# Performance work log

Hardware: AMD Instinct MI355X
Metric: run time of the kernel (lower is better)

The kernel has to match this reference:

```python
import jax, jax.numpy as jnp
import numpy as np

N_NODES = 50000
N_EDGES = 1600000
D = 128


def setup_inputs() -> dict:
    key = jax.random.key(0)
    ks = jax.random.split(key, 8)
    features = jax.random.normal(ks[0], (N_NODES, D), dtype=jnp.float32)
    edge_src = jax.random.randint(ks[1], (N_EDGES,), 0, N_NODES, dtype=jnp.int32)
    edge_dst = jax.random.randint(ks[2], (N_EDGES,), 0, N_NODES, dtype=jnp.int32)
    edge_weight = jax.random.uniform(ks[3], (N_EDGES,), dtype=jnp.float32)
    scale = 1.0 / np.sqrt(D)
    W1 = jax.random.normal(ks[4], (D, D), dtype=jnp.float32) * scale
    b1 = jnp.zeros((D,), dtype=jnp.float32)
    W2 = jax.random.normal(ks[5], (D, D), dtype=jnp.float32) * scale
    b2 = jnp.zeros((D,), dtype=jnp.float32)
    return {"features": features, "edge_src": edge_src, "edge_dst": edge_dst,
            "edge_weight": edge_weight, "W1": W1, "b1": b1, "W2": W2, "b2": b2}


def _gcn_layer(x, W, b, edge_src, edge_dst, edge_weight, n_nodes):
    # support = X @ W  (dense projection), then spmm: out[d] += w_e * support[s]
    support = x @ W  # [N, D]
    msgs = support[edge_src] * edge_weight[:, None]  # [E, D] gather + scale
    out = jax.ops.segment_sum(msgs, edge_dst, num_segments=n_nodes)  # scatter-add
    return out + b


def reference(features, edge_src, edge_dst, edge_weight, W1, b1, W2, b2):
    h = _gcn_layer(features, W1, b1, edge_src, edge_dst, edge_weight, N_NODES)
    h = jax.nn.relu(h)
    # dropout is identity in eval mode (training=False)
    out = _gcn_layer(h, W2, b2, edge_src, edge_dst, edge_weight, N_NODES)
    return out
```

## Files before the change

kernel.cpp:

```cpp
#include <hip/hip_runtime.h>
#include <hip/hip_fp16.h>
#include <math.h>

#define D 128
#define BSHIFT 7
#define BSIZE (1 << BSHIFT)
#define CHUNK 4096
#define BT 1024
#define CAP 7168
#define BSTR 16
#define LDP 132
#define SENTV 0xFFFFFFFFu

typedef _Float16 half8 __attribute__((ext_vector_type(8)));
typedef float f32x4 __attribute__((ext_vector_type(4)));
typedef float f32x2 __attribute__((ext_vector_type(2)));

#if __has_builtin(__builtin_amdgcn_cvt_pk_f32_fp8) && \
    __has_builtin(__builtin_amdgcn_cvt_pk_fp8_f32)
#define HAVE_FP8_CVT 1
#endif

__device__ __forceinline__ float dec_e4m3(unsigned int b) {
    const unsigned int e = (b >> 3) & 0xF;
    const unsigned int m = b & 7;
    float v;
    if (e == 0) v = (float)m * 0.001953125f;
    else        v = (float)(8 + m) * __uint_as_float((e + 117) << 23);
    return (b & 0x80) ? -v : v;
}

__device__ __forceinline__ unsigned char enc_fp8(float x) {
#ifdef HAVE_FP8_CVT
    return (unsigned char)(__builtin_amdgcn_cvt_pk_fp8_f32(x, x, 0, false) & 0xFF);
#else
    const float ax0 = fabsf(x);
    const unsigned int s = (x < 0.f) ? 0x80u : 0u;
    const float ax = fminf(ax0, 448.0f);
    if (ax < 0.015625f) {
        const int m = __float2int_rn(ax * 512.0f);
        return (unsigned char)(s | (unsigned int)m);
    }
    int ex;
    const float fr = frexpf(ax, &ex);
    int m = __float2int_rn(fr * 16.0f) - 8;
    int e = ex - 1 + 7;
    if (m == 8) { m = 0; e += 1; }
    if (e > 15) return (unsigned char)(s | 0x7E);
    return (unsigned char)(s | ((unsigned int)e << 3) | (unsigned int)m);
#endif
}

__global__ __launch_bounds__(512) void init_misc(int* __restrict__ bcur, int NB,
                                                 const float* __restrict__ W1,
                                                 const float* __restrict__ W2,
                                                 __half* __restrict__ W1t,
                                                 __half* __restrict__ W2t) {
    if (blockIdx.x == 0) {
        const int b = threadIdx.x;
        if (b < NB) bcur[b * BSTR] = b * CAP;
        return;
    }
    const int which = blockIdx.x - 1;
    const float* W = which ? W2 : W1;
    __half* Wt = which ? W2t : W1t;
    for (int i = threadIdx.x; i < D * D; i += 512) {
        const int n = i >> 7, k = i & 127;
        Wt[i] = __float2half(W[k * D + n]);
    }
}

__device__ __forceinline__ void gemm_body_f32(const float* __restrict__ X,
                                              const __half* __restrict__ Wt,
                                              unsigned char* __restrict__ Y,
                                              int M, int bx) {
    const int lane = threadIdx.x & 63;
    const int wv = threadIdx.x >> 6;
    const int row0 = bx * 256 + wv * 16;
    const int m = lane & 15;
    const int q = lane >> 4;

    if (row0 >= M) return;
    const int rsafe = min(row0 + m, M - 1);
    const float4* Xr = (const float4*)(X + (size_t)rsafe * D);
    half8 a[4];
#pragma unroll
    for (int kt = 0; kt < 4; ++kt) {
        const float4 lo = Xr[kt * 8 + q * 2];
        const float4 hi = Xr[kt * 8 + q * 2 + 1];
        a[kt] = (half8){(_Float16)lo.x, (_Float16)lo.y, (_Float16)lo.z,
                        (_Float16)lo.w, (_Float16)hi.x, (_Float16)hi.y,
                        (_Float16)hi.z, (_Float16)hi.w};
    }

    const half8* WT8 = (const half8*)Wt;
#pragma unroll
    for (int ct = 0; ct < 8; ++ct) {
        const int n = ct * 16 + m;
        f32x4 acc = {0.f, 0.f, 0.f, 0.f};
#pragma unroll
        for (int kt = 0; kt < 4; ++kt) {
            const half8 b = WT8[(size_t)n * 16 + kt * 4 + q];
            acc = __builtin_amdgcn_mfma_f32_16x16x32_f16(a[kt], b, acc, 0, 0, 0);
        }
#pragma unroll
        for (int r = 0; r < 4; ++r) {
            const int orow = row0 + q * 4 + r;
            if (orow < M)
                Y[(size_t)orow * D + ct * 16 + m] = enc_fp8(acc[r]);
        }
    }
}

__global__ __launch_bounds__(BT) void scatter_gemm1(const int* __restrict__ src,
                                                    const int* __restrict__ dst,
                                                    const float* __restrict__ wgt,
                                                    int* __restrict__ bcur,
                                                    unsigned int* __restrict__ csrA,
                                                    int E, int NB, int nscat,
                                                    const float* __restrict__ X,
                                                    const __half* __restrict__ W1t,
                                                    unsigned char* __restrict__ sup,
                                                    int M) {
    if (blockIdx.x >= (unsigned)nscat) {
        gemm_body_f32(X, W1t, sup, M, blockIdx.x - nscat);
        return;
    }
    __shared__ int lhist[512];
    __shared__ int lstart[512];
    __shared__ int lcur[512];
    const int tid = threadIdx.x;
    const int base = blockIdx.x * CHUNK;

    for (int b = tid; b < NB; b += BT) lhist[b] = 0;
    __syncthreads();

    int dreg[CHUNK / BT];
#pragma unroll
    for (int u = 0; u < CHUNK / BT; ++u) {
        const int e = base + u * BT + tid;
        dreg[u] = (e < E) ? dst[e] : -1;
        if (dreg[u] >= 0) atomicAdd(&lhist[dreg[u] >> BSHIFT], 1);
    }
    __syncthreads();

    for (int b = tid; b < NB; b += BT) {
        const int c = lhist[b];
        if (c) {
            const int r = atomicAdd(&bcur[b * BSTR], (c + 15) & ~15);
            lstart[b] = r;
            lcur[b] = r;
        }
    }
    __syncthreads();

#pragma unroll
    for (int u = 0; u < CHUNK / BT; ++u) {
        const int d = dreg[u];
        if (d >= 0) {
            const int e = base + u * BT + tid;
            const int b = d >> BSHIFT;
            const int pos = atomicAdd(&lcur[b], 1);
            const unsigned int wq =
                (unsigned int)__float2int_rn(wgt[e] * 511.0f);
            const unsigned int kv = (unsigned int)src[e] |
                                    ((unsigned int)(d & (BSIZE - 1)) << 16) |
                                    (wq << 23);
            if (pos < (b + 1) * CAP) csrA[pos] = kv;
        }
    }
    __syncthreads();

    for (int b = tid; b < NB; b += BT) {
        const int c = lhist[b];
        if (c) {
            const int beg = lstart[b] + c;
            const int fin = lstart[b] + ((c + 15) & ~15);
            for (int p = beg; p < fin; ++p)
                if (p < (b + 1) * CAP) csrA[p] = SENTV;
        }
    }
}

__device__ __forceinline__ void accum8(float acc[8], uint2 raw, float w) {
#ifdef HAVE_FP8_CVT
    const f32x2 f01 = __builtin_amdgcn_cvt_pk_f32_fp8(raw.x, false);
    const f32x2 f23 = __builtin_amdgcn_cvt_pk_f32_fp8(raw.x, true);
    const f32x2 f45 = __builtin_amdgcn_cvt_pk_f32_fp8(raw.y, false);
    const f32x2 f67 = __builtin_amdgcn_cvt_pk_f32_fp8(raw.y, true);
    acc[0] = fmaf(w, f01[0], acc[0]);
    acc[1] = fmaf(w, f01[1], acc[1]);
    acc[2] = fmaf(w, f23[0], acc[2]);
    acc[3] = fmaf(w, f23[1], acc[3]);
    acc[4] = fmaf(w, f45[0], acc[4]);
    acc[5] = fmaf(w, f45[1], acc[5]);
    acc[6] = fmaf(w, f67[0], acc[6]);
    acc[7] = fmaf(w, f67[1], acc[7]);
#else
#pragma unroll
    for (int i = 0; i < 4; ++i)
        acc[i] = fmaf(w, dec_e4m3((raw.x >> (8 * i)) & 0xFF), acc[i]);
#pragma unroll
    for (int i = 0; i < 4; ++i)
        acc[4 + i] = fmaf(w, dec_e4m3((raw.y >> (8 * i)) & 0xFF), acc[4 + i]);
#endif
}

__device__ __forceinline__ float kv_w(unsigned int kv) {
    return (float)(kv >> 23) * (1.0f / 511.0f);
}

__device__ __forceinline__ void gather_row(const uint2* __restrict__ supv,
                                           const unsigned int* __restrict__ csr,
                                           int beg, int end, int l, float acc[8]) {
    int j = beg;
    for (; j + 16 <= end; j += 16) {
        unsigned int kv[16];
        uint2 r[16];
#pragma unroll
        for (int u = 0; u < 16; ++u) kv[u] = csr[j + u];
#pragma unroll
        for (int u = 0; u < 16; ++u)
            r[u] = supv[(size_t)(kv[u] & 0xFFFF) * 16 + l];
#pragma unroll
        for (int u = 0; u < 16; ++u) accum8(acc, r[u], kv_w(kv[u]));
    }
    if (j + 8 <= end) {
        unsigned int kv[8];
        uint2 r[8];
#pragma unroll
        for (int u = 0; u < 8; ++u) kv[u] = csr[j + u];
#pragma unroll
        for (int u = 0; u < 8; ++u)
            r[u] = supv[(size_t)(kv[u] & 0xFFFF) * 16 + l];
#pragma unroll
        for (int u = 0; u < 8; ++u) accum8(acc, r[u], kv_w(kv[u]));
        j += 8;
    }
    if (j + 4 <= end) {
        unsigned int kv[4];
        uint2 r[4];
#pragma unroll
        for (int u = 0; u < 4; ++u) kv[u] = csr[j + u];
#pragma unroll
        for (int u = 0; u < 4; ++u)
            r[u] = supv[(size_t)(kv[u] & 0xFFFF) * 16 + l];
#pragma unroll
        for (int u = 0; u < 4; ++u) accum8(acc, r[u], kv_w(kv[u]));
        j += 4;
    }
    for (; j < end; ++j) {
        const unsigned int kv = csr[j];
        const uint2 r = supv[(size_t)(kv & 0xFFFF) * 16 + l];
        accum8(acc, r, kv_w(kv));
    }
}

__device__ __forceinline__ void gather_row_lds(const uint2* __restrict__ supv,
                                               const unsigned int* ekv2,
                                               int beg, int end, int l, float acc[8]) {
    int j = beg;
    for (; j + 16 <= end; j += 16) {
        unsigned int kv[16];
        uint2 r[16];
#pragma unroll
        for (int u = 0; u < 16; ++u) kv[u] = ekv2[j + u];
#pragma unroll
        for (int u = 0; u < 16; ++u)
            r[u] = supv[(size_t)(kv[u] & 0xFFFF) * 16 + l];
#pragma unroll
        for (int u = 0; u < 16; ++u) accum8(acc, r[u], kv_w(kv[u]));
    }
    if (j + 8 <= end) {
        unsigned int kv[8];
        uint2 r[8];
#pragma unroll
        for (int u = 0; u < 8; ++u) kv[u] = ekv2[j + u];
#pragma unroll
        for (int u = 0; u < 8; ++u)
            r[u] = supv[(size_t)(kv[u] & 0xFFFF) * 16 + l];
#pragma unroll
        for (int u = 0; u < 8; ++u) accum8(acc, r[u], kv_w(kv[u]));
        j += 8;
    }
    if (j + 4 <= end) {
        unsigned int kv[4];
        uint2 r[4];
#pragma unroll
        for (int u = 0; u < 4; ++u) kv[u] = ekv2[j + u];
#pragma unroll
        for (int u = 0; u < 4; ++u)
            r[u] = supv[(size_t)(kv[u] & 0xFFFF) * 16 + l];
#pragma unroll
        for (int u = 0; u < 4; ++u) accum8(acc, r[u], kv_w(kv[u]));
        j += 4;
    }
    for (; j < end; ++j) {
        const unsigned int kv = ekv2[j];
        const uint2 r = supv[(size_t)(kv & 0xFFFF) * 16 + l];
        accum8(acc, r, kv_w(kv));
    }
}

__global__ __launch_bounds__(BT) void gather_sort_gemm(
    const unsigned int* __restrict__ csrA, const int* __restrict__ bcur,
    int* __restrict__ offsets, int* __restrict__ deg,
    unsigned int* __restrict__ csr,
    const unsigned char* __restrict__ sup, const float* __restrict__ b1,
    const __half* __restrict__ W2t, unsigned char* __restrict__ sup2, int M) {
    __shared__ unsigned int ekv2[CAP];
    __shared__ _Float16 hA[BSIZE * LDP];
    __shared__ int hist[BSIZE];
    __shared__ int loff[BSIZE];
    __shared__ int ldeg[BSIZE];
    __shared__ int ncur[BSIZE];
    __shared__ int wtot[2];

    const int b = blockIdx.x;
    const int n0 = b << BSHIFT;
    const int tid = threadIdx.x;
    const int nloc = min(BSIZE, M - n0);
    const int bstart = b * CAP;
    const int bend = min(bcur[b * BSTR], bstart + CAP);

    if (tid < BSIZE) hist[tid] = 0;
    __syncthreads();

    unsigned int reg[CAP / BT];
#pragma unroll
    for (int i = 0; i < CAP / BT; ++i) {
        const int j = bstart + i * BT + tid;
        unsigned int kv = SENTV;
        if (j < bend) kv = csrA[j];
        reg[i] = kv;
        if ((kv & 0xFFFFu) != 0xFFFFu)
            atomicAdd(&hist[(kv >> 16) & (BSIZE - 1)], 1);
    }
    __syncthreads();

    const int lane = tid & 63;
    const int wv = tid >> 6;
    const int v = (tid < BSIZE) ? hist[tid] : 0;
    int incl = v;
#pragma unroll
    for (int off = 1; off < 64; off <<= 1) {
        int t = __shfl_up(incl, off, 64);
        if (lane >= off) incl += t;
    }
    if (tid < BSIZE && lane == 63) wtot[wv] = incl;
    __syncthreads();
    if (tid < BSIZE) {
        const int carry = (wv == 1) ? wtot[0] : 0;
        const int ex = incl - v + carry;
        loff[tid] = ex;
        ldeg[tid] = v;
        ncur[tid] = ex;
        if (tid < nloc) {
            offsets[n0 + tid] = bstart + ex;
            deg[n0 + tid] = v;
        }
    }
    for (int i = tid; i < (BSIZE - nloc) * LDP; i += BT)
        hA[nloc * LDP + i] = (_Float16)0.f;
    __syncthreads();

#pragma unroll
    for (int i = 0; i < CAP / BT; ++i) {
        const unsigned int kv = reg[i];
        if ((kv & 0xFFFFu) != 0xFFFFu) {
            const int pos = atomicAdd(&ncur[(kv >> 16) & (BSIZE - 1)], 1);
            ekv2[pos] = kv;
        }
    }
    __syncthreads();

#pragma unroll
    for (int i = 0; i < CAP / BT; ++i)
        csr[bstart + i * BT + tid] = ekv2[i * BT + tid];

    const int grp = tid >> 4;
    const int l = tid & 15;
    const uint2* supv = (const uint2*)sup;
    const float4 c0 = ((const float4*)b1)[l * 2];
    const float4 c1 = ((const float4*)b1)[l * 2 + 1];
    for (int n = grp; n < nloc; n += 64) {
        float acc[8];
        acc[0] = c0.x; acc[1] = c0.y; acc[2] = c0.z; acc[3] = c0.w;
        acc[4] = c1.x; acc[5] = c1.y; acc[6] = c1.z; acc[7] = c1.w;
        const int beg = loff[n];
        gather_row_lds(supv, ekv2, beg, beg + ldeg[n], l, acc);
        half8 hv;
#pragma unroll
        for (int i = 0; i < 8; ++i) hv[i] = (_Float16)fmaxf(acc[i], 0.f);
        *(half8*)&hA[n * LDP + l * 8] = hv;
    }
    __syncthreads();

    const int m = lane & 15;
    const int qq = lane >> 4;
    const int rt = wv >> 1;
    const int ct0 = (wv & 1) * 4;
    half8 a[4];
#pragma unroll
    for (int kt = 0; kt < 4; ++kt)
        a[kt] = *(const half8*)&hA[(rt * 16 + m) * LDP + kt * 32 + qq * 8];

    const half8* WT8 = (const half8*)W2t;
#pragma unroll
    for (int c = 0; c < 4; ++c) {
        const int ct = ct0 + c;
        const int ncol = ct * 16 + m;
        f32x4 dacc = {0.f, 0.f, 0.f, 0.f};
#pragma unroll
        for (int kt = 0; kt < 4; ++kt) {
            const half8 bb = WT8[(size_t)ncol * 16 + kt * 4 + qq];
            dacc = __builtin_amdgcn_mfma_f32_16x16x32_f16(a[kt], bb, dacc, 0, 0, 0);
        }
#pragma unroll
        for (int r = 0; r < 4; ++r) {
            const int orow = n0 + rt * 16 + qq * 4 + r;
            if (orow < M)
                sup2[(size_t)orow * D + ct * 16 + m] = enc_fp8(dacc[r]);
        }
    }
}

__global__ __launch_bounds__(256) void gather_out(const unsigned char* __restrict__ sup,
                                                  const int* __restrict__ offsets,
                                                  const int* __restrict__ deg,
                                                  const unsigned int* __restrict__ csr,
                                                  const float* __restrict__ bias,
                                                  float* __restrict__ out, int M) {
    const int tid = threadIdx.x;
    const int q = tid >> 4;
    const int l = tid & 15;
    const int n = blockIdx.x * 16 + q;
    if (n >= M) return;

    float acc[8];
    {
        const float4 c0 = ((const float4*)bias)[l * 2];
        const float4 c1 = ((const float4*)bias)[l * 2 + 1];
        acc[0] = c0.x; acc[1] = c0.y; acc[2] = c0.z; acc[3] = c0.w;
        acc[4] = c1.x; acc[5] = c1.y; acc[6] = c1.z; acc[7] = c1.w;
    }
    const int beg = offsets[n];
    gather_row((const uint2*)sup, csr, beg, beg + deg[n], l, acc);

    f32x4* out4 = (f32x4*)out;
    const f32x4 o0 = {acc[0], acc[1], acc[2], acc[3]};
    const f32x4 o1 = {acc[4], acc[5], acc[6], acc[7]};
    __builtin_nontemporal_store(o0, out4 + (size_t)n * 32 + l * 2);
    __builtin_nontemporal_store(o1, out4 + (size_t)n * 32 + l * 2 + 1);
}

extern "C" void kernel_launch(void* const* d_in, const int* in_sizes, int n_in,
                              void* d_out, int out_size, void* d_ws, size_t ws_size,
                              hipStream_t stream) {
    const float* features = (const float*)d_in[0];
    const int*   esrc     = (const int*)d_in[1];
    const int*   edst     = (const int*)d_in[2];
    const float* ew       = (const float*)d_in[3];
    const float* W1       = (const float*)d_in[4];
    const float* b1       = (const float*)d_in[5];
    const float* W2       = (const float*)d_in[6];
    const float* b2       = (const float*)d_in[7];
    float* out = (float*)d_out;

    const int M = in_sizes[0] / D;
    const int E = in_sizes[1];
    const int NB = (M + BSIZE - 1) >> BSHIFT;

    unsigned int* csrA = (unsigned int*)d_ws;
    unsigned int* csr  = csrA + (size_t)NB * CAP;
    unsigned char* sup = (unsigned char*)(csr + (size_t)NB * CAP);
    unsigned char* sup2 = sup + (size_t)M * D;
    int*    offsets = (int*)(sup2 + (size_t)M * D);
    int*    deg     = offsets + M;
    int*    bcur    = deg + M;
    __half* W1t     = (__half*)(bcur + (size_t)NB * BSTR);
    __half* W2t     = W1t + D * D;

    const int gemmb = (M + 255) / 256;
    const int node_blocks = (M + 15) / 16;
    const int nscat = (E + CHUNK - 1) / CHUNK;

    init_misc<<<3, 512, 0, stream>>>(bcur, NB, W1, W2, W1t, W2t);
    scatter_gemm1<<<nscat + gemmb, BT, 0, stream>>>(esrc, edst, ew, bcur, csrA, E,
                                                    NB, nscat, features, W1t, sup, M);
    gather_sort_gemm<<<NB, BT, 0, stream>>>(csrA, bcur, offsets, deg, csr, sup, b1,
                                            W2t, sup2, M);
    gather_out<<<node_blocks, 256, 0, stream>>>(sup2, offsets, deg, csr, b2, out, M);
}
```

Measured before the change: 244.6 us.

## Split second-layer support into column slabs and unfuse scatter from gemm1

Layer-2 support is now stored as two 64-column fp8 slabs, and the final gather runs per slab, each block handling 32 nodes with 8 lanes per node. Each slab is 3.2MB instead of 6.4MB, so the random gathers should stay in cache better. The fused scatter+gemm1 kernel is also split into two launches, with gemm1 using 64-row blocks of 256 threads. The cost is an extra launch, loss of overlap between scatter and gemm, and reading the CSR indices twice in the final gather.

```diff
diff --git a/kernel.cpp b/kernel.cpp
--- a/kernel.cpp
+++ b/kernel.cpp
@@ -10,6 +10,7 @@
 #define CAP 7168
 #define BSTR 16
 #define LDP 132
+#define SLW 64
 #define SENTV 0xFFFFFFFFu
 
 typedef _Float16 half8 __attribute__((ext_vector_type(8)));
@@ -70,62 +71,12 @@
     }
 }
 
-__device__ __forceinline__ void gemm_body_f32(const float* __restrict__ X,
-                                              const __half* __restrict__ Wt,
-                                              unsigned char* __restrict__ Y,
-                                              int M, int bx) {
-    const int lane = threadIdx.x & 63;
-    const int wv = threadIdx.x >> 6;
-    const int row0 = bx * 256 + wv * 16;
-    const int m = lane & 15;
-    const int q = lane >> 4;
-
-    if (row0 >= M) return;
-    const int rsafe = min(row0 + m, M - 1);
-    const float4* Xr = (const float4*)(X + (size_t)rsafe * D);
-    half8 a[4];
-#pragma unroll
-    for (int kt = 0; kt < 4; ++kt) {
-        const float4 lo = Xr[kt * 8 + q * 2];
-        const float4 hi = Xr[kt * 8 + q * 2 + 1];
-        a[kt] = (half8){(_Float16)lo.x, (_Float16)lo.y, (_Float16)lo.z,
-                        (_Float16)lo.w, (_Float16)hi.x, (_Float16)hi.y,
-                        (_Float16)hi.z, (_Float16)hi.w};
-    }
-
-    const half8* WT8 = (const half8*)Wt;
-#pragma unroll
-    for (int ct = 0; ct < 8; ++ct) {
-        const int n = ct * 16 + m;
-        f32x4 acc = {0.f, 0.f, 0.f, 0.f};
-#pragma unroll
-        for (int kt = 0; kt < 4; ++kt) {
-            const half8 b = WT8[(size_t)n * 16 + kt * 4 + q];
-            acc = __builtin_amdgcn_mfma_f32_16x16x32_f16(a[kt], b, acc, 0, 0, 0);
-        }
-#pragma unroll
-        for (int r = 0; r < 4; ++r) {
-            const int orow = row0 + q * 4 + r;
-            if (orow < M)
-                Y[(size_t)orow * D + ct * 16 + m] = enc_fp8(acc[r]);
-        }
-    }
-}
-
-__global__ __launch_bounds__(BT) void scatter_gemm1(const int* __restrict__ src,
-                                                    const int* __restrict__ dst,
-                                                    const float* __restrict__ wgt,
-                                                    int* __restrict__ bcur,
-                                                    unsigned int* __restrict__ csrA,
-                                                    int E, int NB, int nscat,
-                                                    const float* __restrict__ X,
-                                                    const __half* __restrict__ W1t,
-                                                    unsigned char* __restrict__ sup,
-                                                    int M) {
-    if (blockIdx.x >= (unsigned)nscat) {
-        gemm_body_f32(X, W1t, sup, M, blockIdx.x - nscat);
-        return;
-    }
+__global__ __launch_bounds__(BT) void scatter_prep(const int* __restrict__ src,
+                                                   const int* __restrict__ dst,
+                                                   const float* __restrict__ wgt,
+                                                   int* __restrict__ bcur,
+                                                   unsigned int* __restrict__ csrA,
+                                                   int E, int NB) {
     __shared__ int lhist[512];
     __shared__ int lstart[512];
     __shared__ int lcur[512];
@@ -178,6 +129,47 @@
             const int fin = lstart[b] + ((c + 15) & ~15);
             for (int p = beg; p < fin; ++p)
                 if (p < (b + 1) * CAP) csrA[p] = SENTV;
+        }
+    }
+}
+
+__global__ __launch_bounds__(256) void gemm1(const float* __restrict__ X,
+                                             const __half* __restrict__ Wt,
+                                             unsigned char* __restrict__ Y, int M) {
+    const int lane = threadIdx.x & 63;
+    const int wv = threadIdx.x >> 6;
+    const int row0 = blockIdx.x * 64 + wv * 16;
+    const int m = lane & 15;
+    const int q = lane >> 4;
+
+    if (row0 >= M) return;
+    const int rsafe = min(row0 + m, M - 1);
+    const float4* Xr = (const float4*)(X + (size_t)rsafe * D);
+    half8 a[4];
+#pragma unroll
+    for (int kt = 0; kt < 4; ++kt) {
+        const float4 lo = Xr[kt * 8 + q * 2];
+        const float4 hi = Xr[kt * 8 + q * 2 + 1];
+        a[kt] = (half8){(_Float16)lo.x, (_Float16)lo.y, (_Float16)lo.z,
+                        (_Float16)lo.w, (_Float16)hi.x, (_Float16)hi.y,
+                        (_Float16)hi.z, (_Float16)hi.w};
+    }
+
+    const half8* WT8 = (const half8*)Wt;
+#pragma unroll
+    for (int ct = 0; ct < 8; ++ct) {
+        const int n = ct * 16 + m;
+        f32x4 acc = {0.f, 0.f, 0.f, 0.f};
+#pragma unroll
+        for (int kt = 0; kt < 4; ++kt) {
+            const half8 b = WT8[(size_t)n * 16 + kt * 4 + q];
+            acc = __builtin_amdgcn_mfma_f32_16x16x32_f16(a[kt], b, acc, 0, 0, 0);
+        }
+#pragma unroll
+        for (int r = 0; r < 4; ++r) {
+            const int orow = row0 + q * 4 + r;
+            if (orow < M)
+                Y[(size_t)orow * D + ct * 16 + m] = enc_fp8(acc[r]);
         }
     }
 }
@@ -210,52 +202,6 @@
     return (float)(kv >> 23) * (1.0f / 511.0f);
 }
 
-__device__ __forceinline__ void gather_row(const uint2* __restrict__ supv,
-                                           const unsigned int* __restrict__ csr,
-                                           int beg, int end, int l, float acc[8]) {
-    int j = beg;
-    for (; j + 16 <= end; j += 16) {
-        unsigned int kv[16];
-        uint2 r[16];
-#pragma unroll
-        for (int u = 0; u < 16; ++u) kv[u] = csr[j + u];
-#pragma unroll
-        for (int u = 0; u < 16; ++u)
-            r[u] = supv[(size_t)(kv[u] & 0xFFFF) * 16 + l];
-#pragma unroll
-        for (int u = 0; u < 16; ++u) accum8(acc, r[u], kv_w(kv[u]));
-    }
-    if (j + 8 <= end) {
-        unsigned int kv[8];
-        uint2 r[8];
-#pragma unroll
-        for (int u = 0; u < 8; ++u) kv[u] = csr[j + u];
-#pragma unroll
-        for (int u = 0; u < 8; ++u)
-            r[u] = supv[(size_t)(kv[u] & 0xFFFF) * 16 + l];
-#pragma unroll
-        for (int u = 0; u < 8; ++u) accum8(acc, r[u], kv_w(kv[u]));
-        j += 8;
-    }
-    if (j + 4 <= end) {
-        unsigned int kv[4];
-        uint2 r[4];
-#pragma unroll
-        for (int u = 0; u < 4; ++u) kv[u] = csr[j + u];
-#pragma unroll
-        for (int u = 0; u < 4; ++u)
-            r[u] = supv[(size_t)(kv[u] & 0xFFFF) * 16 + l];
-#pragma unroll
-        for (int u = 0; u < 4; ++u) accum8(acc, r[u], kv_w(kv[u]));
-        j += 4;
-    }
-    for (; j < end; ++j) {
-        const unsigned int kv = csr[j];
-        const uint2 r = supv[(size_t)(kv & 0xFFFF) * 16 + l];
-        accum8(acc, r, kv_w(kv));
-    }
-}
-
 __device__ __forceinline__ void gather_row_lds(const uint2* __restrict__ supv,
                                                const unsigned int* ekv2,
                                                int beg, int end, int l, float acc[8]) {
@@ -299,6 +245,51 @@
         const unsigned int kv = ekv2[j];
         const uint2 r = supv[(size_t)(kv & 0xFFFF) * 16 + l];
         accum8(acc, r, kv_w(kv));
+    }
+}
+
+__device__ __forceinline__ void gather_row_sl(const uint2* __restrict__ supv,
+                                              const unsigned int* __restrict__ csr,
+                                              int beg, int end, int p, float acc[8]) {
+    int j = beg;
+    for (; j + 16 <= end; j += 16) {
+        unsigned int kv[16];
+        uint2 r[16];
+#pragma unroll
+        for (int u = 0; u < 16; ++u) kv[u] = csr[j + u];
+#pragma unroll
+        for (int u = 0; u < 16; ++u)
+            r[u] = supv[(size_t)(kv[u] & 0xFFFF) * 8 + p];
+#pragma unroll
+        for (int u = 0; u < 16; ++u) accum8(acc, r[u], kv_w(kv[u]));
+    }
+    if (j + 8 <= end) {
+        unsigned int kv[8];
+        uint2 r[8];
+#pragma unroll
+        for (int u = 0; u < 8; ++u) kv[u] = csr[j + u];
+#pragma unroll
+        for (int u = 0; u < 8; ++u)
+            r[u] = supv[(size_t)(kv[u] & 0xFFFF) * 8 + p];
+#pragma unroll
+        for (int u = 0; u < 8; ++u) accum8(acc, r[u], kv_w(kv[u]));
+        j += 8;
+    }
+    if (j + 4 <= end) {
+        unsigned int kv[4];
+        uint2 r[4];
+#pragma unroll
+        for (int u = 0; u < 4; ++u) kv[u] = csr[j + u];
+#pragma unroll
+        for (int u = 0; u < 4; ++u)
+            r[u] = supv[(size_t)(kv[u] & 0xFFFF) * 8 + p];
+#pragma unroll
+        for (int u = 0; u < 4; ++u) accum8(acc, r[u], kv_w(kv[u]));
+        j += 4;
+    }
+    for (; j < end; ++j) {
+        const unsigned int kv = csr[j];
+        accum8(acc, supv[(size_t)(kv & 0xFFFF) * 8 + p], kv_w(kv));
     }
 }
 
@@ -420,38 +411,42 @@
         for (int r = 0; r < 4; ++r) {
             const int orow = n0 + rt * 16 + qq * 4 + r;
             if (orow < M)
-                sup2[(size_t)orow * D + ct * 16 + m] = enc_fp8(dacc[r]);
-        }
-    }
-}
-
-__global__ __launch_bounds__(256) void gather_out(const unsigned char* __restrict__ sup,
+                sup2[(size_t)(ct >> 2) * M * SLW + (size_t)orow * SLW +
+                     (ct & 3) * 16 + m] = enc_fp8(dacc[r]);
+        }
+    }
+}
+
+__global__ __launch_bounds__(256) void gather2_sl(const unsigned char* __restrict__ sup,
                                                   const int* __restrict__ offsets,
                                                   const int* __restrict__ deg,
                                                   const unsigned int* __restrict__ csr,
                                                   const float* __restrict__ bias,
                                                   float* __restrict__ out, int M) {
+    const int sl = blockIdx.x & 1;
+    const int nb = blockIdx.x >> 1;
     const int tid = threadIdx.x;
-    const int q = tid >> 4;
-    const int l = tid & 15;
-    const int n = blockIdx.x * 16 + q;
+    const int g = tid >> 3;
+    const int p = tid & 7;
+    const int n = nb * 32 + g;
     if (n >= M) return;
 
     float acc[8];
     {
-        const float4 c0 = ((const float4*)bias)[l * 2];
-        const float4 c1 = ((const float4*)bias)[l * 2 + 1];
+        const float4 c0 = ((const float4*)bias)[sl * 16 + p * 2];
+        const float4 c1 = ((const float4*)bias)[sl * 16 + p * 2 + 1];
         acc[0] = c0.x; acc[1] = c0.y; acc[2] = c0.z; acc[3] = c0.w;
         acc[4] = c1.x; acc[5] = c1.y; acc[6] = c1.z; acc[7] = c1.w;
     }
+    const uint2* supv = (const uint2*)(sup + (size_t)sl * M * SLW);
     const int beg = offsets[n];
-    gather_row((const uint2*)sup, csr, beg, beg + deg[n], l, acc);
-
-    f32x4* out4 = (f32x4*)out;
+    gather_row_sl(supv, csr, beg, beg + deg[n], p, acc);
+
+    f32x4* out4 = (f32x4*)(out + (size_t)n * D + sl * SLW + p * 8);
     const f32x4 o0 = {acc[0], acc[1], acc[2], acc[3]};
     const f32x4 o1 = {acc[4], acc[5], acc[6], acc[7]};
-    __builtin_nontemporal_store(o0, out4 + (size_t)n * 32 + l * 2);
-    __builtin_nontemporal_store(o1, out4 + (size_t)n * 32 + l * 2 + 1);
+    __builtin_nontemporal_store(o0, out4);
+    __builtin_nontemporal_store(o1, out4 + 1);
 }
 
 extern "C" void kernel_launch(void* const* d_in, const int* in_sizes, int n_in,
@@ -481,14 +476,14 @@
     __half* W1t     = (__half*)(bcur + (size_t)NB * BSTR);
     __half* W2t     = W1t + D * D;
 
-    const int gemmb = (M + 255) / 256;
-    const int node_blocks = (M + 15) / 16;
+    const int nb64 = (M + 63) / 64;
+    const int nb32 = (M + 31) / 32;
     const int nscat = (E + CHUNK - 1) / CHUNK;
 
     init_misc<<<3, 512, 0, stream>>>(bcur, NB, W1, W2, W1t, W2t);
-    scatter_gemm1<<<nscat + gemmb, BT, 0, stream>>>(esrc, edst, ew, bcur, csrA, E,
-                                                    NB, nscat, features, W1t, sup, M);
+    scatter_prep<<<nscat, BT, 0, stream>>>(esrc, edst, ew, bcur, csrA, E, NB);
+    gemm1<<<nb64, 256, 0, stream>>>(features, W1t, sup, M);
     gather_sort_gemm<<<NB, BT, 0, stream>>>(csrA, bcur, offsets, deg, csr, sup, b1,
                                             W2t, sup2, M);
-    gather_out<<<node_blocks, 256, 0, stream>>>(sup2, offsets, deg, csr, b2, out, M);
-}
+    gather2_sl<<<2 * nb32, 256, 0, stream>>>(sup2, offsets, deg, csr, b2, out, M);
+}
```

Result: faster. 234.1 us (-4.3%).
